# Kernel optimization log

Hardware: AMD Instinct MI355X
Metric: run time of the kernel (lower is better)

The kernel has to match this reference:

```python
import jax, jax.numpy as jnp
import numpy as np

N_HIDDEN = 2048
N_HEADS = 64
EXPAND = 2
D_STATE = 128
D_CONV = 4
CHUNK = 128
DT_MIN = 0.001
DT_MAX = 0.1
INNER = EXPAND * N_HIDDEN            # 4096
HEAD_DIM = INNER // N_HEADS          # 64
CONV_DIM = INNER + 2 * D_STATE       # 4352
D_IN_PROJ = 2 * INNER + 2 * D_STATE + N_HEADS  # 8512
EPS = 1e-6


def setup_inputs() -> dict:
    key = jax.random.key(0)
    ks = jax.random.split(key, 10)
    B, L = 2, 2048
    s = lambda fan_in: 1.0 / np.sqrt(fan_in)
    return {
        "x": jax.random.normal(ks[0], (B, L, N_HIDDEN), jnp.float32),
        "W_in": jax.random.normal(ks[1], (N_HIDDEN, D_IN_PROJ), jnp.float32) * s(N_HIDDEN),
        "b_in": jnp.zeros((D_IN_PROJ,), jnp.float32),
        "conv_w": jax.random.normal(ks[2], (D_CONV, 1, CONV_DIM), jnp.float32) * s(D_CONV),
        "conv_b": jnp.zeros((CONV_DIM,), jnp.float32),
        "A_log": jnp.log(jnp.arange(1, N_HEADS + 1, dtype=jnp.float32)),
        "dt_bias": jax.random.normal(ks[3], (N_HEADS,), jnp.float32) * 0.1,
        "D_param": jnp.ones((N_HEADS,), jnp.float32),
        "norm_w": jnp.ones((INNER,), jnp.float32),
        "W_out": jax.random.normal(ks[4], (INNER, N_HIDDEN), jnp.float32) * s(INNER),
        "b_out": jnp.zeros((N_HIDDEN,), jnp.float32),
    }


def _segsum(x):
    t = x.shape[-1]
    cs = jnp.cumsum(x, axis=-1)
    seg = cs[..., :, None] - cs[..., None, :]
    mask = jnp.tril(jnp.ones((t, t), dtype=bool))
    return jnp.where(mask, seg, -jnp.inf)


def _ssd(x, dt, a, b_mat, c_mat, d, dt_bias):
    # x: (B,L,H,P)  dt: (B,L,H)  a: (H,)  b_mat/c_mat: (B,L,H,N)  d: (H,)
    bsz, seq, h, p = x.shape
    dt = jnp.clip(jax.nn.softplus(dt + dt_bias), DT_MIN, DT_MAX)
    d_res = d.reshape(1, 1, h, 1) * x
    x_disc = x * dt[..., None]
    a_disc = a * dt                                   # (B,L,H)
    ch = lambda t_: t_.reshape(bsz, seq // CHUNK, CHUNK, *t_.shape[2:])
    x_blk, b_blk, c_blk = ch(x_disc), ch(b_mat), ch(c_mat)
    a_blk = jnp.transpose(ch(a_disc), (0, 3, 1, 2))   # (B,H,C,Lc)
    a_cum = jnp.cumsum(a_blk, axis=-1)
    l_mat = jnp.exp(_segsum(a_blk))                   # (B,H,C,Lc,Lc)
    y_diag = jnp.einsum("bclhn,bcshn,bhcls,bcshp->bclhp", c_blk, b_blk, l_mat, x_blk)
    decay_states = jnp.exp(a_cum[..., -1:] - a_cum)
    states = jnp.einsum("bclhn,bhcl,bclhp->bchpn", b_blk, decay_states, x_blk)
    states = jnp.concatenate([jnp.zeros_like(states[:, :1]), states], axis=1)
    a_end = jnp.pad(a_cum[..., -1], ((0, 0), (0, 0), (1, 0)))
    decay_chunk = jnp.exp(_segsum(a_end))
    new_states = jnp.einsum("bhzc,bchpn->bzhpn", decay_chunk, states)
    states = new_states[:, :-1]
    y_off = jnp.einsum("bclhn,bchpn,bhcl->bclhp", c_blk, states, jnp.exp(a_cum))
    y = (y_diag + y_off).reshape(bsz, seq, h, p)
    return y + d_res


def reference(x, W_in, b_in, conv_w, conv_b, A_log, dt_bias, D_param, norm_w, W_out, b_out):
    B, L, _ = x.shape
    zxbcdt = x @ W_in + b_in
    z = zxbcdt[..., :INNER]
    xBC = zxbcdt[..., INNER:INNER + CONV_DIM]
    dt = zxbcdt[..., -N_HEADS:]
    # causal depthwise conv1d + silu
    xp = jnp.pad(xBC, ((0, 0), (D_CONV - 1, 0), (0, 0)))
    xBC = jax.lax.conv_general_dilated(
        xp, conv_w, window_strides=(1,), padding="VALID",
        dimension_numbers=("NWC", "WIO", "NWC"), feature_group_count=CONV_DIM,
    ) + conv_b
    xBC = jax.nn.silu(xBC)
    x_ssm = xBC[..., :INNER].reshape(B, L, N_HEADS, HEAD_DIM)
    b_mat = jnp.broadcast_to(xBC[..., INNER:INNER + D_STATE][:, :, None, :], (B, L, N_HEADS, D_STATE))
    c_mat = jnp.broadcast_to(xBC[..., INNER + D_STATE:][:, :, None, :], (B, L, N_HEADS, D_STATE))
    a = -jnp.exp(A_log)
    y = _ssd(x_ssm, dt, a, b_mat, c_mat, D_param, dt_bias)
    y = y.reshape(B, L, INNER)
    # gated RMSNorm
    y = y * jax.nn.silu(z)
    y = y * jax.lax.rsqrt(jnp.mean(y * y, axis=-1, keepdims=True) + EPS) * norm_w
    return y @ W_out + b_out
```

## Files before the change

kernel.cpp:

```cpp
#include <hip/hip_runtime.h>
#include <hip/hip_bf16.h>
#include <cstdint>

typedef __bf16 bf16x8 __attribute__((ext_vector_type(8)));
typedef __bf16 bf16x4 __attribute__((ext_vector_type(4)));
typedef float  f4     __attribute__((ext_vector_type(4)));

constexpr int BATCH   = 2;
constexpr int LSEQ    = 2048;
constexpr int NH      = 2048;
constexpr int INNER   = 4096;
constexpr int DSTATE  = 128;
constexpr int CONVD   = 4352;
constexpr int HEADS   = 64;
constexpr int HDIM    = 64;
constexpr int NPROJ   = 8512;
constexpr int NPROJ_P = 8704;
constexpr int NC      = 16;
constexpr int CH      = 128;
constexpr int ROWS    = BATCH * LSEQ;
constexpr int NBC     = BATCH * NC;

__device__ __forceinline__ f4 f4zero() { f4 v; v.x=0.f; v.y=0.f; v.z=0.f; v.w=0.f; return v; }

__device__ __forceinline__ void gload16(const __bf16* g, const char* l) {
    __builtin_amdgcn_global_load_lds((const __attribute__((address_space(1))) void*)g,
                                     (__attribute__((address_space(3))) void*)l, 16, 0, 0);
}

__global__ __launch_bounds__(256) void k_cast_bf16(const float* __restrict__ in,
                                                   __bf16* __restrict__ out, int n4) {
    int i = blockIdx.x * 256 + threadIdx.x;
    if (i >= n4) return;
    f4 v = ((const f4*)in)[i];
    bf16x4 o;
    o[0] = (__bf16)v.x; o[1] = (__bf16)v.y; o[2] = (__bf16)v.z; o[3] = (__bf16)v.w;
    ((bf16x4*)out)[i] = o;
}

__global__ __launch_bounds__(256) void k_transpose_cast(const float* __restrict__ in,
                                                        __bf16* __restrict__ out,
                                                        int R, int C, int Cp) {
    __shared__ float tile[32][33];
    int bn = blockIdx.x * 32, bk = blockIdx.y * 32;
    int tx = threadIdx.x & 31, ty = threadIdx.x >> 5;
#pragma unroll
    for (int i = 0; i < 4; ++i) {
        int k = bk + ty + i * 8, n = bn + tx;
        tile[ty + i * 8][tx] = (k < R && n < C) ? in[(size_t)k * C + n] : 0.f;
    }
    __syncthreads();
#pragma unroll
    for (int i = 0; i < 4; ++i) {
        int n = bn + ty + i * 8, k = bk + tx;
        if (n < Cp && k < R) out[(size_t)n * R + k] = (__bf16)tile[tx][ty + i * 8];
    }
}

template<int BM, int BN, int WM, int WN, int EPI>
__global__ __launch_bounds__(512, 2) void k_gemm8(
    const __bf16* __restrict__ A, const __bf16* __restrict__ Bt,
    const float* __restrict__ bias, float* __restrict__ Cf,
    __bf16* __restrict__ zf, __bf16* __restrict__ xbcpre, float* __restrict__ dtraw,
    int N, int K, int gridY) {
    extern __shared__ char smem[];
    constexpr int MFRAG = BM / (WM * 16);
    constexpr int NFRAG = BN / (WN * 16);
    constexpr int ALINES = BM / 64, BLINES = BN / 64, LT = ALINES + BLINES;
    constexpr int ABYTES = BM * 128, BUFB = ABYTES + BN * 128;
    constexpr int LPPA = BM / 128, LPPB = BN / 128;

    int tid = threadIdx.x, lane = tid & 63, w = tid >> 6;
    int wm = w / WN, wn = w % WN;

    int bid = blockIdx.x;
    int q = gridDim.x >> 3;
    int wg = (bid & 7) * q + (bid >> 3);
    int bx = wg / gridY, by = wg - bx * gridY;
    int mBase = by * BM, nBase = bx * BN;

    int rl = lane & 15, rq = lane >> 4;
    int kslp = rq ^ (((rl >> 3) & 1) << 1);
    const int rdA = (wm * MFRAG * 16 + rl) * 64 + kslp * 16;
    const int rdB = ABYTES + (wn * NFRAG * 16 + rl) * 64 + kslp * 16;

    int lanep = lane ^ (((lane >> 5) & 1) << 1);
    int srs = lanep >> 2, sksl = lanep & 3;

    const __bf16* sA[ALINES];
#pragma unroll
    for (int li = 0; li < ALINES; ++li)
        sA[li] = A + (size_t)(mBase + (li % LPPA) * 128 + w * 16 + srs) * K + (li / LPPA) * 32 + sksl * 8;
    const __bf16* sB[BLINES];
#pragma unroll
    for (int li = 0; li < BLINES; ++li)
        sB[li] = Bt + (size_t)(nBase + (li % LPPB) * 128 + w * 16 + srs) * K + (li / LPPB) * 32 + sksl * 8;

    auto stage = [&](int buf, int line, int kt) {
        if (line < ALINES) {
            gload16(sA[line] + kt, smem + buf * BUFB + line * 8192 + w * 1024);
        } else {
            int lb = line - ALINES;
            gload16(sB[lb] + kt, smem + buf * BUFB + ABYTES + lb * 8192 + w * 1024);
        }
    };

    bf16x8 a0[MFRAG], b0[NFRAG], a1[MFRAG], b1[NFRAG];
    auto ldregs = [&](int bufoff, int ks, bf16x8* ar, bf16x8* br) {
#pragma unroll
        for (int i = 0; i < MFRAG; ++i)
            ar[i] = *(const bf16x8*)(smem + bufoff + ks * (BM * 64) + rdA + i * 1024);
#pragma unroll
        for (int i = 0; i < NFRAG; ++i)
            br[i] = *(const bf16x8*)(smem + bufoff + ks * (BN * 64) + rdB + i * 1024);
    };

    f4 acc[MFRAG][NFRAG];
#pragma unroll
    for (int i = 0; i < MFRAG; ++i)
#pragma unroll
        for (int j = 0; j < NFRAG; ++j) acc[i][j] = f4zero();

    auto domfma = [&](bf16x8* ar, bf16x8* br) {
        __builtin_amdgcn_s_setprio(1);
#pragma unroll
        for (int mi = 0; mi < MFRAG; ++mi)
#pragma unroll
            for (int ni = 0; ni < NFRAG; ++ni)
                acc[mi][ni] = __builtin_amdgcn_mfma_f32_16x16x32_bf16(ar[mi], br[ni], acc[mi][ni], 0, 0, 0);
        __builtin_amdgcn_s_setprio(0);
    };

    const int nt = K >> 6;
#pragma unroll
    for (int li = 0; li < LT; ++li) stage(0, li, 0);
#pragma unroll
    for (int li = 0; li < 4; ++li) stage(1, li, 64);
    asm volatile("s_waitcnt vmcnt(4)" ::: "memory");
    __builtin_amdgcn_s_barrier();
    ldregs(0, 0, a0, b0);

    for (int t = 0; t < nt; ++t) {
        const int cur = t & 1;
        const int bufoff = cur * BUFB;
        ldregs(bufoff, 1, a1, b1);
        if (t + 1 < nt) {
#pragma unroll
            for (int li = 4; li < LT; ++li) stage(cur ^ 1, li, (t + 1) << 6);
        }
        __builtin_amdgcn_sched_barrier(0);
        domfma(a0, b0);
        asm volatile("s_waitcnt lgkmcnt(0)" ::: "memory");
        __builtin_amdgcn_sched_barrier(0);
        __builtin_amdgcn_s_barrier();
        if (t + 2 < nt) {
#pragma unroll
            for (int li = 0; li < 4; ++li) stage(cur, li, (t + 2) << 6);
        }
        __builtin_amdgcn_sched_barrier(0);
        domfma(a1, b1);
        if (t + 1 < nt) {
            if (t + 2 < nt) {
                asm volatile("s_waitcnt vmcnt(4)" ::: "memory");
            } else {
                asm volatile("s_waitcnt vmcnt(0)" ::: "memory");
            }
            __builtin_amdgcn_s_barrier();
            ldregs((cur ^ 1) * BUFB, 0, a0, b0);
        }
    }

    int cl = lane & 15, rq4 = (lane >> 4) * 4;
#pragma unroll
    for (int nf = 0; nf < NFRAG; ++nf) {
        int col0 = nBase + wn * NFRAG * 16 + nf * 16;
        int col = col0 + cl;
        if constexpr (EPI == 1) {
            if (col0 >= NPROJ) continue;
            float bvv = bias[col];
#pragma unroll
            for (int mf = 0; mf < MFRAG; ++mf) {
#pragma unroll
                for (int j = 0; j < 4; ++j) {
                    int row = mBase + wm * MFRAG * 16 + mf * 16 + rq4 + j;
                    float v = acc[mf][nf][j] + bvv;
                    if (col0 < INNER) {
                        zf[(size_t)row * INNER + col] = (__bf16)v;
                    } else if (col0 < INNER + CONVD) {
                        xbcpre[(size_t)row * CONVD + (col - INNER)] = (__bf16)v;
                    } else {
                        dtraw[(size_t)row * HEADS + (col - INNER - CONVD)] = v;
                    }
                }
            }
        } else {
            float bvv = bias[col];
#pragma unroll
            for (int mf = 0; mf < MFRAG; ++mf)
#pragma unroll
                for (int j = 0; j < 4; ++j) {
                    int row = mBase + wm * MFRAG * 16 + mf * 16 + rq4 + j;
                    Cf[(size_t)row * N + col] = acc[mf][nf][j] + bvv;
                }
        }
    }
}

__global__ __launch_bounds__(256) void k_conv_silu(const __bf16* __restrict__ xbcpre,
                                                   const float* __restrict__ conv_w,
                                                   const float* __restrict__ conv_b,
                                                   __bf16* __restrict__ xbc) {
    int idx = blockIdx.x * 256 + threadIdx.x;
    int c8 = idx % (CONVD / 8);
    int bl = idx / (CONVD / 8);
    int l = bl & (LSEQ - 1);
    int c0 = c8 * 8;
    float acc[8];
    const f4* cb4 = (const f4*)(conv_b + c0);
    f4 b0 = cb4[0], b1 = cb4[1];
#pragma unroll
    for (int k = 0; k < 4; ++k) { acc[k] = b0[k]; acc[k + 4] = b1[k]; }
#pragma unroll
    for (int j = 0; j < 4; ++j) {
        int l2 = l + j - 3;
        if (l2 < 0) continue;
        bf16x8 xv = *(const bf16x8*)(xbcpre + (size_t)(bl + j - 3) * CONVD + c0);
        const f4* w4 = (const f4*)(conv_w + j * CONVD + c0);
        f4 w0 = w4[0], w1 = w4[1];
#pragma unroll
        for (int k = 0; k < 4; ++k) {
            acc[k]     += w0[k] * (float)xv[k];
            acc[k + 4] += w1[k] * (float)xv[k + 4];
        }
    }
    bf16x8 o;
#pragma unroll
    for (int k = 0; k < 8; ++k) {
        float a = acc[k];
        o[k] = (__bf16)(a / (1.f + expf(-a)));
    }
    *(bf16x8*)(xbc + (size_t)bl * CONVD + c0) = o;
}

__global__ __launch_bounds__(256) void k_dt(const float* __restrict__ dtraw,
                                            const float* __restrict__ dt_bias,
                                            float* __restrict__ dtp_t) {
    int idx = blockIdx.x * 256 + threadIdx.x;
    int h = idx & 63;
    int bl = idx >> 6;
    int b = bl >> 11, l = bl & (LSEQ - 1);
    float raw = dtraw[idx] + dt_bias[h];
    float sp = raw > 20.f ? raw : log1pf(expf(raw));
    dtp_t[((size_t)(b * HEADS + h)) * LSEQ + l] = fminf(fmaxf(sp, 0.001f), 0.1f);
}

__global__ __launch_bounds__(256) void k_transpose_bc(const __bf16* __restrict__ xbc,
                                                      __bf16* __restrict__ xT,
                                                      __bf16* __restrict__ BtG) {
    int bid = blockIdx.x;
    int ct = bid % 66;
    int rt = (bid / 66) & 1;
    int bc = bid / 132;
    __shared__ float T[64][65];
    int t = threadIdx.x;
    int lr0 = t >> 3, cg = t & 7;
#pragma unroll
    for (int it = 0; it < 2; ++it) {
        int lr = lr0 + it * 32;
        bf16x8 v = *(const bf16x8*)(xbc + (size_t)(bc * CH + rt * 64 + lr) * CONVD + ct * 64 + cg * 8);
#pragma unroll
        for (int j = 0; j < 8; ++j) T[lr][cg * 8 + j] = (float)v[j];
    }
    __syncthreads();
#pragma unroll
    for (int it = 0; it < 2; ++it) {
        int cl = lr0 + it * 32;
        int c = ct * 64 + cl;
        bf16x8 o;
#pragma unroll
        for (int j = 0; j < 8; ++j) o[j] = (__bf16)T[cg * 8 + j][cl];
        __bf16* dst = (c < INNER)
            ? xT  + ((size_t)bc * INNER + c) * CH + rt * 64 + cg * 8
            : BtG + ((size_t)bc * DSTATE + (c - INNER)) * CH + rt * 64 + cg * 8;
        *(bf16x8*)dst = o;
    }
}

__global__ __launch_bounds__(256) void k_cb(const __bf16* __restrict__ xbc,
                                            float* __restrict__ cbT) {
    int bid = blockIdx.x;
    int lg = bid & 7, bc = bid >> 3;
    int tid = threadIdx.x;
    int e0 = lg * 2048 + tid * 8;
    int l = e0 >> 7;
    int s0 = e0 & 127;
    const __bf16* Crow = xbc + (size_t)(bc * CH + l) * CONVD + INNER + DSTATE;
    const __bf16* B0   = xbc + (size_t)(bc * CH + s0) * CONVD + INNER;
    float acc[8];
#pragma unroll
    for (int j = 0; j < 8; ++j) acc[j] = 0.f;
    for (int n8 = 0; n8 < 16; ++n8) {
        bf16x8 cv = *(const bf16x8*)(Crow + n8 * 8);
        float cf[8];
#pragma unroll
        for (int k = 0; k < 8; ++k) cf[k] = (float)cv[k];
#pragma unroll
        for (int j = 0; j < 8; ++j) {
            bf16x8 bvv = *(const bf16x8*)(B0 + (size_t)j * CONVD + n8 * 8);
#pragma unroll
            for (int k = 0; k < 8; ++k) acc[j] += cf[k] * (float)bvv[k];
        }
    }
    float* dst = cbT + ((size_t)bc << 14) + (l << 7) + s0;
#pragma unroll
    for (int j = 0; j < 8; ++j) dst[j] = (s0 + j <= l) ? acc[j] : 0.f;
}

__global__ __launch_bounds__(256) void k_states(const __bf16* __restrict__ xT,
                                                const __bf16* __restrict__ BtG,
                                                const float* __restrict__ dtp_t,
                                                const float* __restrict__ A_log,
                                                __bf16* __restrict__ states,
                                                float* __restrict__ acum_buf,
                                                float* __restrict__ aend_buf) {
    int bid = blockIdx.x;
    int h = bid & 63, c = (bid >> 6) & 15, b = bid >> 10;
    int bc = b * NC + c, bh = b * HEADS + h;
    int tid = threadIdx.x;
    int lane = tid & 63, w = tid >> 6;
    __shared__ __bf16 Ab[64 * 136];
    __shared__ __bf16 Bb[128 * 136];
    __shared__ float s_ac[128], s_dt[128], s_e[128];
    float a_h = -expf(A_log[h]);

    if (tid < 128) {
        float d = dtp_t[(size_t)bh * LSEQ + c * CH + tid];
        s_dt[tid] = d;
        s_ac[tid] = a_h * d;
    }
    __syncthreads();
    for (int offd = 1; offd < 128; offd <<= 1) {
        float v = 0.f;
        if (tid < 128 && tid >= offd) v = s_ac[tid - offd];
        __syncthreads();
        if (tid < 128) s_ac[tid] += v;
        __syncthreads();
    }
    float aend = s_ac[127];
    if (tid < 128) {
        s_e[tid] = expf(aend - s_ac[tid]) * s_dt[tid];
        acum_buf[((size_t)bh * NC + c) * CH + tid] = s_ac[tid];
    }
    if (tid == 0) aend_buf[bh * NC + c] = aend;
    __syncthreads();

    const __bf16* xrow = xT + ((size_t)bc * INNER + h * HDIM) * CH;
#pragma unroll
    for (int it = 0; it < 4; ++it) {
        int task = it * 256 + tid;
        int p = task >> 4, lg2 = task & 15;
        bf16x8 v = *(const bf16x8*)(xrow + (size_t)p * CH + lg2 * 8);
        bf16x8 o;
#pragma unroll
        for (int j = 0; j < 8; ++j) o[j] = (__bf16)((float)v[j] * s_e[lg2 * 8 + j]);
        *(bf16x8*)&Ab[p * 136 + lg2 * 8] = o;
    }
    const __bf16* brow = BtG + (size_t)bc * DSTATE * CH;
#pragma unroll
    for (int it = 0; it < 8; ++it) {
        int task = it * 256 + tid;
        int n = task >> 4, lg2 = task & 15;
        *(bf16x8*)&Bb[n * 136 + lg2 * 8] = *(const bf16x8*)(brow + (size_t)n * CH + lg2 * 8);
    }
    __syncthreads();

    int rl = lane & 15, kq = (lane >> 4) * 8, rq = lane >> 4;
    f4 acc[8];
#pragma unroll
    for (int i = 0; i < 8; ++i) acc[i] = f4zero();
#pragma unroll
    for (int ks = 0; ks < 4; ++ks) {
        int k0 = ks * 32;
        bf16x8 a = *(const bf16x8*)&Ab[(w * 16 + rl) * 136 + k0 + kq];
#pragma unroll
        for (int nf = 0; nf < 8; ++nf) {
            bf16x8 bfr = *(const bf16x8*)&Bb[(nf * 16 + rl) * 136 + k0 + kq];
            acc[nf] = __builtin_amdgcn_mfma_f32_16x16x32_bf16(a, bfr, acc[nf], 0, 0, 0);
        }
    }
    __syncthreads();
#pragma unroll
    for (int nf = 0; nf < 8; ++nf)
#pragma unroll
        for (int j = 0; j < 4; ++j)
            Ab[(w * 16 + rq * 4 + j) * 136 + nf * 16 + rl] = (__bf16)acc[nf][j];
    __syncthreads();
    __bf16* sbase = states + ((size_t)(bc * HEADS + h)) * (HDIM * DSTATE);
#pragma unroll
    for (int it = 0; it < 4; ++it) {
        int task = it * 256 + tid;
        int p = task >> 4, ng = task & 15;
        *(bf16x8*)(sbase + (size_t)p * DSTATE + ng * 8) = *(const bf16x8*)&Ab[p * 136 + ng * 8];
    }
}

__global__ __launch_bounds__(128) void k_scan(__bf16* __restrict__ states,
                                              const float* __restrict__ aend_buf) {
    int s = blockIdx.x & 7;
    int bh = blockIdx.x >> 3;
    int b = bh >> 6, h = bh & 63;
    int tid = threadIdx.x;
    size_t off = (size_t)s * 1024 + (size_t)tid * 8;
    float run[8];
#pragma unroll
    for (int j = 0; j < 8; ++j) run[j] = 0.f;
    for (int c = 0; c < NC; ++c) {
        float dec = expf(aend_buf[bh * NC + c]);
        __bf16* base = states + ((size_t)((b * NC + c) * HEADS + h)) * (HDIM * DSTATE) + off;
        bf16x8 sv = *(bf16x8*)base;
        bf16x8 o;
#pragma unroll
        for (int j = 0; j < 8; ++j) o[j] = (__bf16)run[j];
        *(bf16x8*)base = o;
#pragma unroll
        for (int j = 0; j < 8; ++j) run[j] = run[j] * dec + (float)sv[j];
    }
}

__global__ __launch_bounds__(256) void k_out(const __bf16* __restrict__ xbc,
                                             const __bf16* __restrict__ xT,
                                             const float* __restrict__ dtp_t,
                                             const float* __restrict__ cbT,
                                             const __bf16* __restrict__ prev,
                                             const float* __restrict__ acum_buf,
                                             const float* __restrict__ D_param,
                                             __bf16* __restrict__ ybuf) {
    int bid = blockIdx.x;
    int h = bid & 63, c = (bid >> 6) & 15, b = bid >> 10;
    int bc = b * NC + c, bh = b * HEADS + h;
    int tid = threadIdx.x;
    int lane = tid & 63, w = tid >> 6;
    __shared__ __bf16 Ab[128 * 136];
    __shared__ __bf16 Bb[64 * 136];
    __shared__ float s_ac[128], s_dt[128];
    if (tid < 128) {
        s_ac[tid] = acum_buf[((size_t)bh * NC + c) * CH + tid];
        s_dt[tid] = dtp_t[(size_t)bh * LSEQ + c * CH + tid];
    }

#pragma unroll
    for (int it = 0; it < 8; ++it) {
        int task = it * 256 + tid;
        int l = task >> 4, ng = task & 15;
        *(bf16x8*)&Ab[l * 136 + ng * 8] =
            *(const bf16x8*)(xbc + (size_t)(bc * CH + l) * CONVD + INNER + DSTATE + ng * 8);
    }
    const __bf16* pbase = prev + ((size_t)(bc * HEADS + h)) * (HDIM * DSTATE);
#pragma unroll
    for (int it = 0; it < 4; ++it) {
        int task = it * 256 + tid;
        int p = task >> 4, ng = task & 15;
        *(bf16x8*)&Bb[p * 136 + ng * 8] = *(const bf16x8*)(pbase + (size_t)p * DSTATE + ng * 8);
    }
    __syncthreads();

    int rl = lane & 15, kq = (lane >> 4) * 8, rq = lane >> 4;
    f4 acc[2][4];
#pragma unroll
    for (int i = 0; i < 2; ++i)
#pragma unroll
        for (int j = 0; j < 4; ++j) acc[i][j] = f4zero();

#pragma unroll
    for (int ks = 0; ks < 4; ++ks) {
        int k0 = ks * 32;
        bf16x8 a0 = *(const bf16x8*)&Ab[(w * 32 + rl) * 136 + k0 + kq];
        bf16x8 a1 = *(const bf16x8*)&Ab[(w * 32 + 16 + rl) * 136 + k0 + kq];
#pragma unroll
        for (int nf = 0; nf < 4; ++nf) {
            bf16x8 bfr = *(const bf16x8*)&Bb[(nf * 16 + rl) * 136 + k0 + kq];
            acc[0][nf] = __builtin_amdgcn_mfma_f32_16x16x32_bf16(a0, bfr, acc[0][nf], 0, 0, 0);
            acc[1][nf] = __builtin_amdgcn_mfma_f32_16x16x32_bf16(a1, bfr, acc[1][nf], 0, 0, 0);
        }
    }
#pragma unroll
    for (int mf = 0; mf < 2; ++mf)
#pragma unroll
        for (int j = 0; j < 4; ++j) {
            float el = expf(s_ac[w * 32 + mf * 16 + rq * 4 + j]);
#pragma unroll
            for (int nf = 0; nf < 4; ++nf) acc[mf][nf][j] *= el;
        }
    __syncthreads();

    const float* cbb = cbT + ((size_t)bc << 14);
#pragma unroll
    for (int it = 0; it < 8; ++it) {
        int task = it * 256 + tid;
        int l = task >> 4, sg = task & 15;
        int s0 = sg * 8;
        const f4* cv4 = (const f4*)(cbb + (l << 7) + s0);
        f4 c0 = cv4[0], c1 = cv4[1];
        float acl = s_ac[l];
        bf16x8 o;
#pragma unroll
        for (int j = 0; j < 8; ++j) {
            int s = s0 + j;
            float cj = (j < 4) ? c0[j] : c1[j - 4];
            float m = 0.f;
            if (s <= l) m = cj * expf(acl - s_ac[s]) * s_dt[s];
            o[j] = (__bf16)m;
        }
        *(bf16x8*)&Ab[l * 136 + s0] = o;
    }
    const __bf16* xrow = xT + ((size_t)bc * INNER + h * HDIM) * CH;
#pragma unroll
    for (int it = 0; it < 4; ++it) {
        int task = it * 256 + tid;
        int p = task >> 4, lg2 = task & 15;
        *(bf16x8*)&Bb[p * 136 + lg2 * 8] = *(const bf16x8*)(xrow + (size_t)p * CH + lg2 * 8);
    }
    __syncthreads();

#pragma unroll
    for (int ks = 0; ks < 4; ++ks) {
        int k0 = ks * 32;
        bf16x8 a0 = *(const bf16x8*)&Ab[(w * 32 + rl) * 136 + k0 + kq];
        bf16x8 a1 = *(const bf16x8*)&Ab[(w * 32 + 16 + rl) * 136 + k0 + kq];
#pragma unroll
        for (int nf = 0; nf < 4; ++nf) {
            bf16x8 bfr = *(const bf16x8*)&Bb[(nf * 16 + rl) * 136 + k0 + kq];
            acc[0][nf] = __builtin_amdgcn_mfma_f32_16x16x32_bf16(a0, bfr, acc[0][nf], 0, 0, 0);
            acc[1][nf] = __builtin_amdgcn_mfma_f32_16x16x32_bf16(a1, bfr, acc[1][nf], 0, 0, 0);
        }
    }
    __syncthreads();

    float* yT = (float*)Ab;
#pragma unroll
    for (int mf = 0; mf < 2; ++mf)
#pragma unroll
        for (int nf = 0; nf < 4; ++nf)
#pragma unroll
            for (int j = 0; j < 4; ++j)
                yT[(w * 32 + mf * 16 + rq * 4 + j) * 68 + nf * 16 + rl] = acc[mf][nf][j];
    __syncthreads();

    float dh = D_param[h];
#pragma unroll
    for (int it = 0; it < 4; ++it) {
        int task = it * 256 + tid;
        int l = task >> 3, pg = task & 7;
        const f4* yv4 = (const f4*)&yT[l * 68 + pg * 8];
        f4 y0 = yv4[0], y1 = yv4[1];
        bf16x8 xv = *(const bf16x8*)(xbc + (size_t)(bc * CH + l) * CONVD + h * HDIM + pg * 8);
        bf16x8 o;
#pragma unroll
        for (int j = 0; j < 4; ++j) {
            o[j]     = (__bf16)(y0[j] + dh * (float)xv[j]);
            o[j + 4] = (__bf16)(y1[j] + dh * (float)xv[j + 4]);
        }
        *(bf16x8*)(ybuf + (size_t)(bc * CH + l) * INNER + h * HDIM + pg * 8) = o;
    }
}

__global__ __launch_bounds__(256) void k_gate_norm(__bf16* __restrict__ ybuf,
                                                   const __bf16* __restrict__ zf,
                                                   const float* __restrict__ norm_w) {
    int row = blockIdx.x, tid = threadIdx.x;
    bf16x8* yrow = (bf16x8*)(ybuf + (size_t)row * INNER);
    const bf16x8* zrow = (const bf16x8*)(zf + (size_t)row * INNER);
    float v[2][8];
    float ss = 0.f;
#pragma unroll
    for (int i = 0; i < 2; ++i) {
        bf16x8 yv = yrow[i * 256 + tid];
        bf16x8 zv = zrow[i * 256 + tid];
#pragma unroll
        for (int j = 0; j < 8; ++j) {
            float z = (float)zv[j];
            float t = (float)yv[j] * (z / (1.f + expf(-z)));
            v[i][j] = t;
            ss += t * t;
        }
    }
#pragma unroll
    for (int off = 32; off > 0; off >>= 1) ss += __shfl_down(ss, off, 64);
    __shared__ float red[4];
    __shared__ float scs;
    if ((tid & 63) == 0) red[tid >> 6] = ss;
    __syncthreads();
    if (tid == 0) scs = rsqrtf((red[0] + red[1] + red[2] + red[3]) * (1.f / INNER) + 1e-6f);
    __syncthreads();
    float scale = scs;
#pragma unroll
    for (int i = 0; i < 2; ++i) {
        const f4* nw = (const f4*)(norm_w + (i * 256 + tid) * 8);
        f4 w0 = nw[0], w1 = nw[1];
        bf16x8 o;
#pragma unroll
        for (int j = 0; j < 4; ++j) {
            o[j]     = (__bf16)(v[i][j]     * scale * w0[j]);
            o[j + 4] = (__bf16)(v[i][j + 4] * scale * w1[j]);
        }
        yrow[i * 256 + tid] = o;
    }
}

extern "C" void kernel_launch(void* const* d_in, const int* in_sizes, int n_in,
                              void* d_out, int out_size, void* d_ws, size_t ws_size,
                              hipStream_t stream) {
    const float* x       = (const float*)d_in[0];
    const float* W_in    = (const float*)d_in[1];
    const float* b_in    = (const float*)d_in[2];
    const float* conv_w  = (const float*)d_in[3];
    const float* conv_b  = (const float*)d_in[4];
    const float* A_log   = (const float*)d_in[5];
    const float* dt_bias = (const float*)d_in[6];
    const float* D_par   = (const float*)d_in[7];
    const float* norm_w  = (const float*)d_in[8];
    const float* W_out   = (const float*)d_in[9];
    const float* b_out   = (const float*)d_in[10];
    float* out = (float*)d_out;

    char* ws = (char*)d_ws;
    constexpr size_t SZ_XBF    = (size_t)ROWS * NH * 2;
    constexpr size_t SZ_WTIN   = (size_t)NPROJ_P * NH * 2;
    constexpr size_t SZ_R1     = SZ_XBF + SZ_WTIN;
    constexpr size_t SZ_ZF     = (size_t)ROWS * INNER * 2;
    constexpr size_t SZ_XBC    = (size_t)ROWS * CONVD * 2;
    constexpr size_t SZ_STATES = (size_t)NBC * HEADS * HDIM * DSTATE * 2;
    constexpr size_t SZ_CBT    = (size_t)NBC * CH * CH * 4;
    constexpr size_t SZ_ACUM   = (size_t)BATCH * HEADS * NC * CH * 4;
    constexpr size_t SZ_AEND   = (size_t)BATCH * HEADS * NC * 4;
    constexpr size_t SZ_DTP    = (size_t)ROWS * HEADS * 4;

    __bf16* xbf    = (__bf16*)(ws);
    __bf16* wtin   = (__bf16*)(ws + SZ_XBF);
    __bf16* zf     = (__bf16*)(ws + SZ_R1);
    __bf16* xbcpre = (__bf16*)(ws + SZ_R1 + SZ_ZF);
    __bf16* xbc    = (__bf16*)(ws + SZ_R1 + SZ_ZF + SZ_XBC);
    float*  dtraw  = (float*) (ws + SZ_R1 + SZ_ZF + 2 * SZ_XBC);
    __bf16* states = (__bf16*)(ws);
    float*  cbT    = (float*) (ws + SZ_STATES);
    float*  acum   = (float*) (ws + SZ_STATES + SZ_CBT);
    float*  aend   = (float*) (ws + SZ_STATES + SZ_CBT + SZ_ACUM);
    float*  dtp_t  = (float*) (ws + SZ_STATES + SZ_CBT + SZ_ACUM + SZ_AEND);
    __bf16* BtG    = (__bf16*)(ws + SZ_STATES + SZ_CBT + SZ_ACUM + SZ_AEND + SZ_DTP);
    __bf16* ybuf   = xbcpre;
    __bf16* wtout  = xbc;
    __bf16* xT     = (__bf16*)out;

    (void)ws_size; (void)in_sizes; (void)n_in; (void)out_size;

    hipFuncSetAttribute(reinterpret_cast<const void*>(&k_gemm8<256,256,2,4,1>),
                        hipFuncAttributeMaxDynamicSharedMemorySize, 131072);
    hipFuncSetAttribute(reinterpret_cast<const void*>(&k_gemm8<256,128,4,2,0>),
                        hipFuncAttributeMaxDynamicSharedMemorySize, 98304);

    k_cast_bf16<<<(ROWS * NH / 4 + 255) / 256, 256, 0, stream>>>(x, xbf, ROWS * NH / 4);
    k_transpose_cast<<<dim3(NPROJ_P / 32, NH / 32), 256, 0, stream>>>(W_in, wtin, NH, NPROJ, NPROJ_P);

    k_gemm8<256,256,2,4,1><<<(NPROJ_P / 256) * (ROWS / 256), 512, 131072, stream>>>(
        xbf, wtin, b_in, nullptr, zf, xbcpre, dtraw, NPROJ_P, NH, ROWS / 256);

    k_conv_silu<<<ROWS * (CONVD / 8) / 256, 256, 0, stream>>>(xbcpre, conv_w, conv_b, xbc);
    k_dt<<<ROWS * HEADS / 256, 256, 0, stream>>>(dtraw, dt_bias, dtp_t);
    k_transpose_bc<<<NBC * 132, 256, 0, stream>>>(xbc, xT, BtG);
    k_cb<<<NBC * 8, 256, 0, stream>>>(xbc, cbT);
    k_states<<<NBC * HEADS, 256, 0, stream>>>(xT, BtG, dtp_t, A_log, states, acum, aend);
    k_scan<<<BATCH * HEADS * 8, 128, 0, stream>>>(states, aend);
    k_out<<<NBC * HEADS, 256, 0, stream>>>(xbc, xT, dtp_t, cbT, states, acum, D_par, ybuf);
    k_gate_norm<<<ROWS, 256, 0, stream>>>(ybuf, zf, norm_w);

    k_transpose_cast<<<dim3(NH / 32, INNER / 32), 256, 0, stream>>>(W_out, wtout, INNER, NH, NH);
    k_gemm8<256,128,4,2,0><<<(NH / 128) * (ROWS / 256), 512, 98304, stream>>>(
        ybuf, wtout, b_out, out, nullptr, nullptr, nullptr, NH, INNER, ROWS / 256);
}
```

Baseline: 460.3 us.

## Use simpler 128x128 in-proj GEMM, trim padding, fuse conv with transpose

The input-projection GEMM moves from the double-buffered 256x256 pipelined kernel to a simple single-buffered 128x128 tile kernel with 256 threads. The padded projection width drops from 8704 to 8576, which wastes fewer columns. The depthwise conv+SiLU kernel now also writes the transposed x and B layouts through shared memory, removing the separate transpose pass that re-read xbc. The simpler GEMM gives up load/compute overlap and register prefetching, and its only gain is less padding waste and more blocks.

```diff
diff --git a/kernel.cpp b/kernel.cpp
--- a/kernel.cpp
+++ b/kernel.cpp
@@ -15,7 +15,7 @@
 constexpr int HEADS   = 64;
 constexpr int HDIM    = 64;
 constexpr int NPROJ   = 8512;
-constexpr int NPROJ_P = 8704;
+constexpr int NPROJ_P = 8576;
 constexpr int NC      = 16;
 constexpr int CH      = 128;
 constexpr int ROWS    = BATCH * LSEQ;
@@ -57,132 +57,76 @@
     }
 }
 
-template<int BM, int BN, int WM, int WN, int EPI>
-__global__ __launch_bounds__(512, 2) void k_gemm8(
+template<int EPI>
+__global__ __launch_bounds__(256) void k_gemm_m97(
     const __bf16* __restrict__ A, const __bf16* __restrict__ Bt,
     const float* __restrict__ bias, float* __restrict__ Cf,
     __bf16* __restrict__ zf, __bf16* __restrict__ xbcpre, float* __restrict__ dtraw,
     int N, int K, int gridY) {
-    extern __shared__ char smem[];
-    constexpr int MFRAG = BM / (WM * 16);
-    constexpr int NFRAG = BN / (WN * 16);
-    constexpr int ALINES = BM / 64, BLINES = BN / 64, LT = ALINES + BLINES;
-    constexpr int ABYTES = BM * 128, BUFB = ABYTES + BN * 128;
-    constexpr int LPPA = BM / 128, LPPB = BN / 128;
+    __shared__ __bf16 As[128 * 32];
+    __shared__ __bf16 Bs[128 * 32];
 
     int tid = threadIdx.x, lane = tid & 63, w = tid >> 6;
-    int wm = w / WN, wn = w % WN;
+    int wm = w >> 1, wn = w & 1;
 
     int bid = blockIdx.x;
     int q = gridDim.x >> 3;
     int wg = (bid & 7) * q + (bid >> 3);
     int bx = wg / gridY, by = wg - bx * gridY;
-    int mBase = by * BM, nBase = bx * BN;
+    int mBase = by * 128, nBase = bx * 128;
 
     int rl = lane & 15, rq = lane >> 4;
     int kslp = rq ^ (((rl >> 3) & 1) << 1);
-    const int rdA = (wm * MFRAG * 16 + rl) * 64 + kslp * 16;
-    const int rdB = ABYTES + (wn * NFRAG * 16 + rl) * 64 + kslp * 16;
+    const int rdA = (wm * 64 + rl) * 64 + kslp * 16;
+    const int rdB = (wn * 64 + rl) * 64 + kslp * 16;
 
     int lanep = lane ^ (((lane >> 5) & 1) << 1);
     int srs = lanep >> 2, sksl = lanep & 3;
 
-    const __bf16* sA[ALINES];
-#pragma unroll
-    for (int li = 0; li < ALINES; ++li)
-        sA[li] = A + (size_t)(mBase + (li % LPPA) * 128 + w * 16 + srs) * K + (li / LPPA) * 32 + sksl * 8;
-    const __bf16* sB[BLINES];
-#pragma unroll
-    for (int li = 0; li < BLINES; ++li)
-        sB[li] = Bt + (size_t)(nBase + (li % LPPB) * 128 + w * 16 + srs) * K + (li / LPPB) * 32 + sksl * 8;
-
-    auto stage = [&](int buf, int line, int kt) {
-        if (line < ALINES) {
-            gload16(sA[line] + kt, smem + buf * BUFB + line * 8192 + w * 1024);
-        } else {
-            int lb = line - ALINES;
-            gload16(sB[lb] + kt, smem + buf * BUFB + ABYTES + lb * 8192 + w * 1024);
-        }
-    };
-
-    bf16x8 a0[MFRAG], b0[NFRAG], a1[MFRAG], b1[NFRAG];
-    auto ldregs = [&](int bufoff, int ks, bf16x8* ar, bf16x8* br) {
-#pragma unroll
-        for (int i = 0; i < MFRAG; ++i)
-            ar[i] = *(const bf16x8*)(smem + bufoff + ks * (BM * 64) + rdA + i * 1024);
-#pragma unroll
-        for (int i = 0; i < NFRAG; ++i)
-            br[i] = *(const bf16x8*)(smem + bufoff + ks * (BN * 64) + rdB + i * 1024);
-    };
-
-    f4 acc[MFRAG][NFRAG];
-#pragma unroll
-    for (int i = 0; i < MFRAG; ++i)
-#pragma unroll
-        for (int j = 0; j < NFRAG; ++j) acc[i][j] = f4zero();
-
-    auto domfma = [&](bf16x8* ar, bf16x8* br) {
-        __builtin_amdgcn_s_setprio(1);
-#pragma unroll
-        for (int mi = 0; mi < MFRAG; ++mi)
-#pragma unroll
-            for (int ni = 0; ni < NFRAG; ++ni)
-                acc[mi][ni] = __builtin_amdgcn_mfma_f32_16x16x32_bf16(ar[mi], br[ni], acc[mi][ni], 0, 0, 0);
-        __builtin_amdgcn_s_setprio(0);
-    };
-
-    const int nt = K >> 6;
-#pragma unroll
-    for (int li = 0; li < LT; ++li) stage(0, li, 0);
-#pragma unroll
-    for (int li = 0; li < 4; ++li) stage(1, li, 64);
-    asm volatile("s_waitcnt vmcnt(4)" ::: "memory");
-    __builtin_amdgcn_s_barrier();
-    ldregs(0, 0, a0, b0);
-
-    for (int t = 0; t < nt; ++t) {
-        const int cur = t & 1;
-        const int bufoff = cur * BUFB;
-        ldregs(bufoff, 1, a1, b1);
-        if (t + 1 < nt) {
-#pragma unroll
-            for (int li = 4; li < LT; ++li) stage(cur ^ 1, li, (t + 1) << 6);
-        }
-        __builtin_amdgcn_sched_barrier(0);
-        domfma(a0, b0);
-        asm volatile("s_waitcnt lgkmcnt(0)" ::: "memory");
-        __builtin_amdgcn_sched_barrier(0);
-        __builtin_amdgcn_s_barrier();
-        if (t + 2 < nt) {
-#pragma unroll
-            for (int li = 0; li < 4; ++li) stage(cur, li, (t + 2) << 6);
-        }
-        __builtin_amdgcn_sched_barrier(0);
-        domfma(a1, b1);
-        if (t + 1 < nt) {
-            if (t + 2 < nt) {
-                asm volatile("s_waitcnt vmcnt(4)" ::: "memory");
-            } else {
-                asm volatile("s_waitcnt vmcnt(0)" ::: "memory");
-            }
-            __builtin_amdgcn_s_barrier();
-            ldregs((cur ^ 1) * BUFB, 0, a0, b0);
-        }
+    const __bf16* gA0 = A  + (size_t)(mBase + w * 16 + srs) * K + sksl * 8;
+    const __bf16* gA1 = gA0 + (size_t)64 * K;
+    const __bf16* gB0 = Bt + (size_t)(nBase + w * 16 + srs) * K + sksl * 8;
+    const __bf16* gB1 = gB0 + (size_t)64 * K;
+
+    f4 acc[4][4];
+#pragma unroll
+    for (int i = 0; i < 4; ++i)
+#pragma unroll
+        for (int j = 0; j < 4; ++j) acc[i][j] = f4zero();
+
+    for (int k0 = 0; k0 < K; k0 += 32) {
+        __syncthreads();
+        gload16(gA0 + k0, (const char*)As + w * 1024);
+        gload16(gA1 + k0, (const char*)As + 4096 + w * 1024);
+        gload16(gB0 + k0, (const char*)Bs + w * 1024);
+        gload16(gB1 + k0, (const char*)Bs + 4096 + w * 1024);
+        __syncthreads();
+        bf16x8 af[4], bf[4];
+#pragma unroll
+        for (int i = 0; i < 4; ++i) {
+            af[i] = *(const bf16x8*)((const char*)As + rdA + i * 1024);
+            bf[i] = *(const bf16x8*)((const char*)Bs + rdB + i * 1024);
+        }
+#pragma unroll
+        for (int mi = 0; mi < 4; ++mi)
+#pragma unroll
+            for (int ni = 0; ni < 4; ++ni)
+                acc[mi][ni] = __builtin_amdgcn_mfma_f32_16x16x32_bf16(af[mi], bf[ni], acc[mi][ni], 0, 0, 0);
     }
 
     int cl = lane & 15, rq4 = (lane >> 4) * 4;
 #pragma unroll
-    for (int nf = 0; nf < NFRAG; ++nf) {
-        int col0 = nBase + wn * NFRAG * 16 + nf * 16;
+    for (int nf = 0; nf < 4; ++nf) {
+        int col0 = nBase + wn * 64 + nf * 16;
         int col = col0 + cl;
         if constexpr (EPI == 1) {
             if (col0 >= NPROJ) continue;
             float bvv = bias[col];
 #pragma unroll
-            for (int mf = 0; mf < MFRAG; ++mf) {
+            for (int mf = 0; mf < 4; ++mf) {
 #pragma unroll
                 for (int j = 0; j < 4; ++j) {
-                    int row = mBase + wm * MFRAG * 16 + mf * 16 + rq4 + j;
+                    int row = mBase + wm * 64 + mf * 16 + rq4 + j;
                     float v = acc[mf][nf][j] + bvv;
                     if (col0 < INNER) {
                         zf[(size_t)row * INNER + col] = (__bf16)v;
@@ -196,50 +140,209 @@
         } else {
             float bvv = bias[col];
 #pragma unroll
-            for (int mf = 0; mf < MFRAG; ++mf)
+            for (int mf = 0; mf < 4; ++mf)
 #pragma unroll
                 for (int j = 0; j < 4; ++j) {
-                    int row = mBase + wm * MFRAG * 16 + mf * 16 + rq4 + j;
+                    int row = mBase + wm * 64 + mf * 16 + rq4 + j;
                     Cf[(size_t)row * N + col] = acc[mf][nf][j] + bvv;
                 }
         }
     }
 }
 
-__global__ __launch_bounds__(256) void k_conv_silu(const __bf16* __restrict__ xbcpre,
-                                                   const float* __restrict__ conv_w,
-                                                   const float* __restrict__ conv_b,
-                                                   __bf16* __restrict__ xbc) {
-    int idx = blockIdx.x * 256 + threadIdx.x;
-    int c8 = idx % (CONVD / 8);
-    int bl = idx / (CONVD / 8);
-    int l = bl & (LSEQ - 1);
-    int c0 = c8 * 8;
-    float acc[8];
+template<int BM, int BN, int WM, int WN>
+__global__ __launch_bounds__(512, 2) void k_gemm8(
+    const __bf16* __restrict__ A, const __bf16* __restrict__ Bt,
+    const float* __restrict__ bias, float* __restrict__ Cf,
+    int N, int K, int gridY) {
+    extern __shared__ char smem[];
+    constexpr int MFRAG = BM / (WM * 16);
+    constexpr int NFRAG = BN / (WN * 16);
+    constexpr int ALINES = BM / 64, BLINES = BN / 64, LT = ALINES + BLINES;
+    constexpr int ABYTES = BM * 128, BUFB = ABYTES + BN * 128;
+    constexpr int LPPA = BM / 128, LPPB = BN / 128;
+
+    int tid = threadIdx.x, lane = tid & 63, w = tid >> 6;
+    int wm = w / WN, wn = w % WN;
+
+    int bid = blockIdx.x;
+    int q = gridDim.x >> 3;
+    int wg = (bid & 7) * q + (bid >> 3);
+    int bx = wg / gridY, by = wg - bx * gridY;
+    int mBase = by * BM, nBase = bx * BN;
+
+    int rl = lane & 15, rq = lane >> 4;
+    int kslp = rq ^ (((rl >> 3) & 1) << 1);
+    const int rdA = (wm * MFRAG * 16 + rl) * 64 + kslp * 16;
+    const int rdB = ABYTES + (wn * NFRAG * 16 + rl) * 64 + kslp * 16;
+
+    int lanep = lane ^ (((lane >> 5) & 1) << 1);
+    int srs = lanep >> 2, sksl = lanep & 3;
+
+    const __bf16* sA[ALINES];
+#pragma unroll
+    for (int li = 0; li < ALINES; ++li)
+        sA[li] = A + (size_t)(mBase + (li % LPPA) * 128 + w * 16 + srs) * K + (li / LPPA) * 32 + sksl * 8;
+    const __bf16* sB[BLINES];
+#pragma unroll
+    for (int li = 0; li < BLINES; ++li)
+        sB[li] = Bt + (size_t)(nBase + (li % LPPB) * 128 + w * 16 + srs) * K + (li / LPPB) * 32 + sksl * 8;
+
+    auto stage = [&](int buf, int line, int kt) {
+        if (line < ALINES) {
+            gload16(sA[line] + kt, smem + buf * BUFB + line * 8192 + w * 1024);
+        } else {
+            int lb = line - ALINES;
+            gload16(sB[lb] + kt, smem + buf * BUFB + ABYTES + lb * 8192 + w * 1024);
+        }
+    };
+
+    bf16x8 a0[MFRAG], b0[NFRAG], a1[MFRAG], b1[NFRAG];
+    auto ldregs = [&](int bufoff, int ks, bf16x8* ar, bf16x8* br) {
+#pragma unroll
+        for (int i = 0; i < MFRAG; ++i)
+            ar[i] = *(const bf16x8*)(smem + bufoff + ks * (BM * 64) + rdA + i * 1024);
+#pragma unroll
+        for (int i = 0; i < NFRAG; ++i)
+            br[i] = *(const bf16x8*)(smem + bufoff + ks * (BN * 64) + rdB + i * 1024);
+    };
+
+    f4 acc[MFRAG][NFRAG];
+#pragma unroll
+    for (int i = 0; i < MFRAG; ++i)
+#pragma unroll
+        for (int j = 0; j < NFRAG; ++j) acc[i][j] = f4zero();
+
+    auto domfma = [&](bf16x8* ar, bf16x8* br) {
+        __builtin_amdgcn_s_setprio(1);
+#pragma unroll
+        for (int mi = 0; mi < MFRAG; ++mi)
+#pragma unroll
+            for (int ni = 0; ni < NFRAG; ++ni)
+                acc[mi][ni] = __builtin_amdgcn_mfma_f32_16x16x32_bf16(ar[mi], br[ni], acc[mi][ni], 0, 0, 0);
+        __builtin_amdgcn_s_setprio(0);
+    };
+
+    const int nt = K >> 6;
+#pragma unroll
+    for (int li = 0; li < LT; ++li) stage(0, li, 0);
+#pragma unroll
+    for (int li = 0; li < 4; ++li) stage(1, li, 64);
+    asm volatile("s_waitcnt vmcnt(4)" ::: "memory");
+    __builtin_amdgcn_s_barrier();
+    ldregs(0, 0, a0, b0);
+
+    for (int t = 0; t < nt; ++t) {
+        const int cur = t & 1;
+        const int bufoff = cur * BUFB;
+        ldregs(bufoff, 1, a1, b1);
+        if (t + 1 < nt) {
+#pragma unroll
+            for (int li = 4; li < LT; ++li) stage(cur ^ 1, li, (t + 1) << 6);
+        }
+        __builtin_amdgcn_sched_barrier(0);
+        domfma(a0, b0);
+        asm volatile("s_waitcnt lgkmcnt(0)" ::: "memory");
+        __builtin_amdgcn_sched_barrier(0);
+        __builtin_amdgcn_s_barrier();
+        if (t + 2 < nt) {
+#pragma unroll
+            for (int li = 0; li < 4; ++li) stage(cur, li, (t + 2) << 6);
+        }
+        __builtin_amdgcn_sched_barrier(0);
+        domfma(a1, b1);
+        if (t + 1 < nt) {
+            if (t + 2 < nt) {
+                asm volatile("s_waitcnt vmcnt(4)" ::: "memory");
+            } else {
+                asm volatile("s_waitcnt vmcnt(0)" ::: "memory");
+            }
+            __builtin_amdgcn_s_barrier();
+            ldregs((cur ^ 1) * BUFB, 0, a0, b0);
+        }
+    }
+
+    int cl = lane & 15, rq4 = (lane >> 4) * 4;
+#pragma unroll
+    for (int nf = 0; nf < NFRAG; ++nf) {
+        int col = nBase + wn * NFRAG * 16 + nf * 16 + cl;
+        float bvv = bias[col];
+#pragma unroll
+        for (int mf = 0; mf < MFRAG; ++mf)
+#pragma unroll
+            for (int j = 0; j < 4; ++j) {
+                int row = mBase + wm * MFRAG * 16 + mf * 16 + rq4 + j;
+                Cf[(size_t)row * N + col] = acc[mf][nf][j] + bvv;
+            }
+    }
+}
+
+__global__ __launch_bounds__(256) void k_conv_tr(const __bf16* __restrict__ xbcpre,
+                                                 const float* __restrict__ conv_w,
+                                                 const float* __restrict__ conv_b,
+                                                 __bf16* __restrict__ xbc,
+                                                 __bf16* __restrict__ xT,
+                                                 __bf16* __restrict__ BtG) {
+    int bid = blockIdx.x;
+    int ct = bid % 68;
+    int rt = (bid / 68) & 1;
+    int bc = bid / 136;
+    __shared__ float T[64][65];
+    int t = threadIdx.x;
+    int lr0 = t >> 3, cg = t & 7;
+    int c0 = ct * 64 + cg * 8;
+
     const f4* cb4 = (const f4*)(conv_b + c0);
-    f4 b0 = cb4[0], b1 = cb4[1];
-#pragma unroll
-    for (int k = 0; k < 4; ++k) { acc[k] = b0[k]; acc[k + 4] = b1[k]; }
+    f4 cb0 = cb4[0], cb1 = cb4[1];
+    f4 w0[4], w1[4];
 #pragma unroll
     for (int j = 0; j < 4; ++j) {
-        int l2 = l + j - 3;
-        if (l2 < 0) continue;
-        bf16x8 xv = *(const bf16x8*)(xbcpre + (size_t)(bl + j - 3) * CONVD + c0);
         const f4* w4 = (const f4*)(conv_w + j * CONVD + c0);
-        f4 w0 = w4[0], w1 = w4[1];
-#pragma unroll
-        for (int k = 0; k < 4; ++k) {
-            acc[k]     += w0[k] * (float)xv[k];
-            acc[k + 4] += w1[k] * (float)xv[k + 4];
-        }
-    }
-    bf16x8 o;
-#pragma unroll
-    for (int k = 0; k < 8; ++k) {
-        float a = acc[k];
-        o[k] = (__bf16)(a / (1.f + expf(-a)));
-    }
-    *(bf16x8*)(xbc + (size_t)bl * CONVD + c0) = o;
+        w0[j] = w4[0]; w1[j] = w4[1];
+    }
+
+#pragma unroll
+    for (int it = 0; it < 2; ++it) {
+        int lr = lr0 + it * 32;
+        int bl = bc * CH + rt * 64 + lr;
+        int l = bl & (LSEQ - 1);
+        float acc[8];
+#pragma unroll
+        for (int k = 0; k < 4; ++k) { acc[k] = cb0[k]; acc[k + 4] = cb1[k]; }
+#pragma unroll
+        for (int j = 0; j < 4; ++j) {
+            if (l + j - 3 < 0) continue;
+            bf16x8 xv = *(const bf16x8*)(xbcpre + (size_t)(bl + j - 3) * CONVD + c0);
+#pragma unroll
+            for (int k = 0; k < 4; ++k) {
+                acc[k]     += w0[j][k] * (float)xv[k];
+                acc[k + 4] += w1[j][k] * (float)xv[k + 4];
+            }
+        }
+        bf16x8 o;
+#pragma unroll
+        for (int k = 0; k < 8; ++k) {
+            float a = acc[k];
+            float s = a / (1.f + expf(-a));
+            o[k] = (__bf16)s;
+            T[lr][cg * 8 + k] = s;
+        }
+        *(bf16x8*)(xbc + (size_t)bl * CONVD + c0) = o;
+    }
+    if (ct >= 66) return;
+    __syncthreads();
+#pragma unroll
+    for (int it = 0; it < 2; ++it) {
+        int cl = lr0 + it * 32;
+        int c = ct * 64 + cl;
+        bf16x8 o;
+#pragma unroll
+        for (int j = 0; j < 8; ++j) o[j] = (__bf16)T[cg * 8 + j][cl];
+        __bf16* dst = (c < INNER)
+            ? xT  + ((size_t)bc * INNER + c) * CH + rt * 64 + cg * 8
+            : BtG + ((size_t)bc * DSTATE + (c - INNER)) * CH + rt * 64 + cg * 8;
+        *(bf16x8*)dst = o;
+    }
 }
 
 __global__ __launch_bounds__(256) void k_dt(const float* __restrict__ dtraw,
@@ -252,38 +355,6 @@
     float raw = dtraw[idx] + dt_bias[h];
     float sp = raw > 20.f ? raw : log1pf(expf(raw));
     dtp_t[((size_t)(b * HEADS + h)) * LSEQ + l] = fminf(fmaxf(sp, 0.001f), 0.1f);
-}
-
-__global__ __launch_bounds__(256) void k_transpose_bc(const __bf16* __restrict__ xbc,
-                                                      __bf16* __restrict__ xT,
-                                                      __bf16* __restrict__ BtG) {
-    int bid = blockIdx.x;
-    int ct = bid % 66;
-    int rt = (bid / 66) & 1;
-    int bc = bid / 132;
-    __shared__ float T[64][65];
-    int t = threadIdx.x;
-    int lr0 = t >> 3, cg = t & 7;
-#pragma unroll
-    for (int it = 0; it < 2; ++it) {
-        int lr = lr0 + it * 32;
-        bf16x8 v = *(const bf16x8*)(xbc + (size_t)(bc * CH + rt * 64 + lr) * CONVD + ct * 64 + cg * 8);
-#pragma unroll
-        for (int j = 0; j < 8; ++j) T[lr][cg * 8 + j] = (float)v[j];
-    }
-    __syncthreads();
-#pragma unroll
-    for (int it = 0; it < 2; ++it) {
-        int cl = lr0 + it * 32;
-        int c = ct * 64 + cl;
-        bf16x8 o;
-#pragma unroll
-        for (int j = 0; j < 8; ++j) o[j] = (__bf16)T[cg * 8 + j][cl];
-        __bf16* dst = (c < INNER)
-            ? xT  + ((size_t)bc * INNER + c) * CH + rt * 64 + cg * 8
-            : BtG + ((size_t)bc * DSTATE + (c - INNER)) * CH + rt * 64 + cg * 8;
-        *(bf16x8*)dst = o;
-    }
 }
 
 __global__ __launch_bounds__(256) void k_cb(const __bf16* __restrict__ xbc,
@@ -653,20 +724,17 @@
 
     (void)ws_size; (void)in_sizes; (void)n_in; (void)out_size;
 
-    hipFuncSetAttribute(reinterpret_cast<const void*>(&k_gemm8<256,256,2,4,1>),
-                        hipFuncAttributeMaxDynamicSharedMemorySize, 131072);
-    hipFuncSetAttribute(reinterpret_cast<const void*>(&k_gemm8<256,128,4,2,0>),
+    hipFuncSetAttribute(reinterpret_cast<const void*>(&k_gemm8<256,128,4,2>),
                         hipFuncAttributeMaxDynamicSharedMemorySize, 98304);
 
     k_cast_bf16<<<(ROWS * NH / 4 + 255) / 256, 256, 0, stream>>>(x, xbf, ROWS * NH / 4);
     k_transpose_cast<<<dim3(NPROJ_P / 32, NH / 32), 256, 0, stream>>>(W_in, wtin, NH, NPROJ, NPROJ_P);
 
-    k_gemm8<256,256,2,4,1><<<(NPROJ_P / 256) * (ROWS / 256), 512, 131072, stream>>>(
-        xbf, wtin, b_in, nullptr, zf, xbcpre, dtraw, NPROJ_P, NH, ROWS / 256);
-
-    k_conv_silu<<<ROWS * (CONVD / 8) / 256, 256, 0, stream>>>(xbcpre, conv_w, conv_b, xbc);
+    k_gemm_m97<1><<<(NPROJ_P / 128) * (ROWS / 128), 256, 0, stream>>>(
+        xbf, wtin, b_in, nullptr, zf, xbcpre, dtraw, NPROJ_P, NH, ROWS / 128);
+
+    k_conv_tr<<<NBC * 136, 256, 0, stream>>>(xbcpre, conv_w, conv_b, xbc, xT, BtG);
     k_dt<<<ROWS * HEADS / 256, 256, 0, stream>>>(dtraw, dt_bias, dtp_t);
-    k_transpose_bc<<<NBC * 132, 256, 0, stream>>>(xbc, xT, BtG);
     k_cb<<<NBC * 8, 256, 0, stream>>>(xbc, cbT);
     k_states<<<NBC * HEADS, 256, 0, stream>>>(xT, BtG, dtp_t, A_log, states, acum, aend);
     k_scan<<<BATCH * HEADS * 8, 128, 0, stream>>>(states, aend);
@@ -674,6 +742,6 @@
     k_gate_norm<<<ROWS, 256, 0, stream>>>(ybuf, zf, norm_w);
 
     k_transpose_cast<<<dim3(NH / 32, INNER / 32), 256, 0, stream>>>(W_out, wtout, INNER, NH, NH);
-    k_gemm8<256,128,4,2,0><<<(NH / 128) * (ROWS / 256), 512, 98304, stream>>>(
-        ybuf, wtout, b_out, out, nullptr, nullptr, nullptr, NH, INNER, ROWS / 256);
-}
+    k_gemm8<256,128,4,2><<<(NH / 128) * (ROWS / 256), 512, 98304, stream>>>(
+        ybuf, wtout, b_out, out, NH, INNER, ROWS / 256);
+}
```

After: 476.8 us. +3.6%, slower.
